# Kernel tuning notes

Measured on AMD Instinct MI355X. Metric: run time of the kernel, lower is better.

The kernel has to match this reference:

```python
import jax, jax.numpy as jnp
import numpy as np

D = 256; NH = 8; NL = 4; NP = 4; DFF = 2048; HD = D // NH
SHAPES = [(64, 64), (32, 32), (16, 16), (8, 8)]
B = 2; LEN = sum(h * w for h, w in SHAPES)


def setup_inputs() -> dict:
    key = jax.random.key(0)
    ks = jax.random.split(key, 12)
    def w(k, shape, s=0.02):
        return jax.random.normal(k, shape, jnp.float32) * s
    starts = np.cumsum([0] + [h * w for h, w in SHAPES[:-1]])
    return {
        "src": jax.random.normal(ks[0], (B, LEN, D), jnp.float32),
        "pos": jax.random.normal(ks[1], (B, LEN, D), jnp.float32) * 0.1,
        "spatial_shapes": jnp.array(SHAPES, dtype=jnp.int32),
        "level_start_index": jnp.array(starts, dtype=jnp.int32),
        "w_value": w(ks[2], (D, D)), "b_value": jnp.zeros((D,), jnp.float32),
        "w_off": w(ks[3], (D, NH * NL * NP * 2)), "b_off": w(ks[4], (NH * NL * NP * 2,), 0.1),
        "w_attn": w(ks[5], (D, NH * NL * NP)), "b_attn": jnp.zeros((NH * NL * NP,), jnp.float32),
        "w_out": w(ks[6], (D, D)), "b_out": jnp.zeros((D,), jnp.float32),
        "w1": w(ks[7], (D, DFF)), "b1": jnp.zeros((DFF,), jnp.float32),
        "w2": w(ks[8], (DFF, D)), "b2": jnp.zeros((D,), jnp.float32),
        "g1": jnp.ones((D,), jnp.float32), "be1": jnp.zeros((D,), jnp.float32),
        "g2": jnp.ones((D,), jnp.float32), "be2": jnp.zeros((D,), jnp.float32),
    }


def _layer_norm(x, g, b):
    mu = jnp.mean(x, -1, keepdims=True)
    v = jnp.var(x, -1, keepdims=True)
    return (x - mu) * jax.lax.rsqrt(v + 1e-5) * g + b


def _reference_points(shapes):
    # torch.linspace(0.5, H-0.5, H)/H == (arange(H)+0.5)/H
    refs = []
    for H, W in shapes:
        ry = (jnp.arange(H, dtype=jnp.float32) + 0.5) / H
        rx = (jnp.arange(W, dtype=jnp.float32) + 0.5) / W
        yy, xx = jnp.meshgrid(ry, rx, indexing='ij')
        refs.append(jnp.stack([xx.ravel(), yy.ravel()], -1))
    return jnp.concatenate(refs, 0)  # (Len, 2) as (x, y)


def _ms_deform_sample(value, loc, shapes):
    # value: (B, Len, NH, HD); loc: (B, Lq, NH, NL, NP, 2) normalized [0,1]
    # Replicates torch grid_sample(bilinear, padding='zeros', align_corners=False).
    Bn, Lq = loc.shape[0], loc.shape[1]
    P = loc.shape[4]
    start = 0
    outs = []
    for lvl, (H, W) in enumerate(shapes):
        v = value[:, start:start + H * W].transpose(0, 2, 1, 3)  # (B, NH, HW, HD)
        start += H * W
        l = loc[:, :, :, lvl]                      # (B, Lq, NH, P, 2)
        x = l[..., 0] * W - 0.5
        y = l[..., 1] * H - 0.5
        x0 = jnp.floor(x); y0 = jnp.floor(y)
        dx = x - x0; dy = y - y0
        x0i = x0.astype(jnp.int32); y0i = y0.astype(jnp.int32)
        acc = None
        for xi, yi, wgt in ((x0i, y0i, (1 - dx) * (1 - dy)),
                            (x0i + 1, y0i, dx * (1 - dy)),
                            (x0i, y0i + 1, (1 - dx) * dy),
                            (x0i + 1, y0i + 1, dx * dy)):
            valid = ((xi >= 0) & (xi < W) & (yi >= 0) & (yi < H)).astype(value.dtype)
            idx = jnp.clip(yi, 0, H - 1) * W + jnp.clip(xi, 0, W - 1)  # (B, Lq, NH, P)
            idx = idx.transpose(0, 2, 1, 3).reshape(Bn, NH, Lq * P)
            g = jnp.take_along_axis(v, idx[..., None], axis=2).reshape(Bn, NH, Lq, P, HD)
            w = (wgt * valid).transpose(0, 2, 1, 3)[..., None]  # (B, NH, Lq, P, 1)
            acc = g * w if acc is None else acc + g * w
        outs.append(acc)  # (B, NH, Lq, P, HD)
    return jnp.stack(outs, 3)  # (B, NH, Lq, NL, NP, HD)


def _forward(src, pos, w_value, b_value, w_off, b_off, w_attn, b_attn,
             w_out, b_out, w1, b1, w2, b2, g1, be1, g2, be2, shapes):
    Bn, Lq, _ = src.shape
    q = src + pos  # with_pos_embed
    value = (src @ w_value + b_value).reshape(Bn, Lq, NH, HD)
    off = (q @ w_off + b_off).reshape(Bn, Lq, NH, NL, NP, 2)
    attn = jax.nn.softmax((q @ w_attn + b_attn).reshape(Bn, Lq, NH, NL * NP), -1)
    attn = attn.reshape(Bn, Lq, NH, NL, NP)
    ref = _reference_points(shapes)  # (Len, 2)
    normalizer = jnp.array([[w_, h_] for h_, w_ in shapes], jnp.float32)  # (NL, 2) = (W, H)
    loc = ref[None, :, None, None, None, :] + off / normalizer[None, None, None, :, None, :]
    sampled = _ms_deform_sample(value, loc, shapes)  # (B, NH, Lq, NL, NP, HD)
    out = jnp.einsum('bqhlp,bhqlpd->bqhd', attn, sampled).reshape(Bn, Lq, D)
    out = out @ w_out + b_out
    x = _layer_norm(src + out, g1, be1)           # residual + norm1
    ff = jax.nn.relu(x @ w1 + b1) @ w2 + b2       # FFN (dropout=0)
    return _layer_norm(x + ff, g2, be2)           # residual + norm2


def reference(src, pos, spatial_shapes, level_start_index, w_value, b_value,
              w_off, b_off, w_attn, b_attn, w_out, b_out, w1, b1, w2, b2,
              g1, be1, g2, be2):
    shapes = [tuple(int(v) for v in s) for s in np.asarray(spatial_shapes)]
    return _forward(src, pos, w_value, b_value, w_off, b_off, w_attn, b_attn,
                    w_out, b_out, w1, b1, w2, b2, g1, be1, g2, be2, shapes)
```

## Files before the change

### kernel.cpp

```cpp
#include <hip/hip_runtime.h>
#include <math.h>

#define D 256
#define NH 8
#define NL 4
#define NP 4
#define DFF 2048
#define HD 32
#define BB 2
#define LEN 5440
#define MROWS (BB * LEN)

typedef __attribute__((ext_vector_type(8))) short short8;
typedef __attribute__((ext_vector_type(4))) float f32x4;
typedef unsigned int uint32;

__device__ __forceinline__ unsigned short f2bf(float f) {
    uint32 u = __float_as_uint(f);
    u += 0x7FFF + ((u >> 16) & 1);
    return (unsigned short)(u >> 16);
}
__device__ __forceinline__ float bf2f(unsigned short h) {
    return __uint_as_float(((uint32)h) << 16);
}
__device__ __forceinline__ uint32 pack2(float a, float b) {
    return (uint32)f2bf(a) | ((uint32)f2bf(b) << 16);
}
__device__ __forceinline__ void acc8(float* a, uint4 u, float w) {
    a[0] += bf2f((unsigned short)u.x) * w; a[1] += bf2f((unsigned short)(u.x >> 16)) * w;
    a[2] += bf2f((unsigned short)u.y) * w; a[3] += bf2f((unsigned short)(u.y >> 16)) * w;
    a[4] += bf2f((unsigned short)u.z) * w; a[5] += bf2f((unsigned short)(u.z >> 16)) * w;
    a[6] += bf2f((unsigned short)u.w) * w; a[7] += bf2f((unsigned short)(u.w >> 16)) * w;
}

__device__ __forceinline__ void gl16(const unsigned short* g, unsigned short* l) {
    __builtin_amdgcn_global_load_lds(
        (const __attribute__((address_space(1))) unsigned int*)g,
        (__attribute__((address_space(3))) unsigned int*)l, 16, 0, 0);
}

__device__ __forceinline__ void swz85(int b, int ncols, int& row, int& col) {
    const int gsz = ncols << 3;
    const int full = 10 * gsz;
    if (b < full) {
        const int g = b / gsz, idx = b - g * gsz;
        row = (g << 3) + (idx & 7);
        col = idx >> 3;
    } else {
        const int idx = b - full;
        row = 80 + idx % 5;
        col = idx / 5;
    }
}

__global__ void prep_a(const float* __restrict__ w_value, const float* __restrict__ w_off,
                       const float* __restrict__ w_attn,
                       const float* __restrict__ b_value, const float* __restrict__ b_off,
                       const float* __restrict__ b_attn,
                       unsigned short* __restrict__ wqvT, float* __restrict__ bqv) {
    __shared__ float tile[32][33];
    const int blk = blockIdx.x;
    const int t = threadIdx.x;
    if (blk >= 160) {
        for (int i = t; i < 640; i += 256)
            bqv[i] = (i < 256) ? b_value[i] : (i < 512 ? b_off[i - 256] : b_attn[i - 512]);
        return;
    }
    const float* W; unsigned short* WT; int N, tid;
    if (blk < 64)       { W = w_value; WT = wqvT;             N = 256; tid = blk; }
    else if (blk < 128) { W = w_off;   WT = wqvT + 256 * 256; N = 256; tid = blk - 64; }
    else                { W = w_attn;  WT = wqvT + 512 * 256; N = 128; tid = blk - 128; }
    const int K = 256;
    const int ntx = N >> 5;
    const int nb = (tid % ntx) * 32, kb = (tid / ntx) * 32;
    const int tx = t & 31, ty = t >> 5;
#pragma unroll
    for (int i = 0; i < 32; i += 8)
        tile[ty + i][tx] = W[(size_t)(kb + ty + i) * N + nb + tx];
    __syncthreads();
#pragma unroll
    for (int i = 0; i < 32; i += 8)
        WT[(size_t)(nb + ty + i) * K + kb + tx] = f2bf(tile[tx][ty + i]);
}

__global__ __launch_bounds__(256) void ffn1_gemm(
        const unsigned short* __restrict__ A,
        const unsigned short* __restrict__ BT, const float* __restrict__ bias,
        unsigned short* __restrict__ Cv, int N, int K, int lda, int ldb) {
    __shared__ unsigned short smraw[17408];
    auto Ash = (unsigned short (*)[128][32])smraw;
    auto Bsh = (unsigned short (*)[128][32])(smraw + 8192);

    int rowt, colt;
    swz85(blockIdx.x, N >> 7, rowt, colt);
    const int row0 = rowt * 128, col0 = colt * 128;

    const int t = threadIdx.x;
    const int wave = t >> 6, lane = t & 63;
    const int wr = wave >> 1, wc = wave & 1;
    const int lrow = lane & 15, quad = lane >> 4;
    const int sr = lane >> 2, sc = (lane & 3) * 8;

    const unsigned short* Ab = A + (size_t)row0 * lda;
    const unsigned short* Bb = BT + (size_t)col0 * ldb;

    f32x4 acc[4][4];
#pragma unroll
    for (int i = 0; i < 4; i++)
#pragma unroll
        for (int j = 0; j < 4; j++) acc[i][j] = (f32x4){0.f, 0.f, 0.f, 0.f};

    auto stage = [&](int buf, int kb) {
#pragma unroll
        for (int j = 0; j < 2; j++) {
            const int r = wave * 32 + j * 16;
            gl16(Ab + (size_t)(r + sr) * lda + kb + sc, &Ash[buf][r][0]);
            gl16(Bb + (size_t)(r + sr) * ldb + kb + sc, &Bsh[buf][r][0]);
        }
    };

    stage(0, 0);
    int i = 0;
    for (int kb = 0; kb < K; kb += 32, ++i) {
        __syncthreads();
        if (kb + 32 < K) stage((i + 1) & 1, kb + 32);
        const int cf = i & 1;
        short8 af[4], bfr[4];
#pragma unroll
        for (int mt = 0; mt < 4; mt++)
            af[mt] = *(const short8*)&Ash[cf][wr * 64 + mt * 16 + lrow][quad * 8];
#pragma unroll
        for (int nt = 0; nt < 4; nt++)
            bfr[nt] = *(const short8*)&Bsh[cf][wc * 64 + nt * 16 + lrow][quad * 8];
#pragma unroll
        for (int mt = 0; mt < 4; mt++)
#pragma unroll
            for (int nt = 0; nt < 4; nt++)
                acc[mt][nt] = __builtin_amdgcn_mfma_f32_16x16x32_bf16(
                    af[mt], bfr[nt], acc[mt][nt], 0, 0, 0);
    }

    __syncthreads();
    auto bounce = (unsigned short (*)[136])smraw;
#pragma unroll
    for (int nt = 0; nt < 4; nt++) {
        const int cl = wc * 64 + nt * 16 + lrow;
        const float bv = bias[col0 + cl];
#pragma unroll
        for (int mt = 0; mt < 4; mt++) {
            f32x4 a = acc[mt][nt];
#pragma unroll
            for (int r = 0; r < 4; r++)
                bounce[wr * 64 + mt * 16 + quad * 4 + r][cl] = f2bf(fmaxf(a[r] + bv, 0.f));
        }
    }
    __syncthreads();
#pragma unroll
    for (int pass = 0; pass < 8; pass++) {
        const int rl = pass * 16 + (t >> 4), ch = t & 15;
        *(uint4*)&Cv[(size_t)(row0 + rl) * N + col0 + ch * 8] =
            *(const uint4*)&bounce[rl][ch * 8];
    }
}

template <int NZ>
__global__ __launch_bounds__(256) void splitk_gemm(
        const unsigned short* __restrict__ A, const unsigned short* __restrict__ BT,
        unsigned short* __restrict__ part, int KC, int lda, int ldb) {
    __shared__ unsigned short smraw[17408];
    auto Ash = (unsigned short (*)[128][32])smraw;
    auto Bsh = (unsigned short (*)[128][32])(smraw + 8192);

    int rowt, cc;
    swz85(blockIdx.x, 2 * NZ, rowt, cc);
    const int row0 = rowt * 128;
    const int col0 = (cc & 1) * 128;
    const int z = cc >> 1;
    const int koff = z * KC;
    unsigned short* __restrict__ C = part + (size_t)z * MROWS * 256;

    const int t = threadIdx.x;
    const int wave = t >> 6, lane = t & 63;
    const int wr = wave >> 1, wc = wave & 1;
    const int lrow = lane & 15, quad = lane >> 4;
    const int sr = lane >> 2, sc = (lane & 3) * 8;

    const unsigned short* Ab = A + (size_t)row0 * lda + koff;
    const unsigned short* Bb = BT + (size_t)col0 * ldb + koff;

    f32x4 acc[4][4];
#pragma unroll
    for (int i = 0; i < 4; i++)
#pragma unroll
        for (int j = 0; j < 4; j++) acc[i][j] = (f32x4){0.f, 0.f, 0.f, 0.f};

    auto stage = [&](int buf, int kb) {
#pragma unroll
        for (int j = 0; j < 2; j++) {
            const int r = wave * 32 + j * 16;
            gl16(Ab + (size_t)(r + sr) * lda + kb + sc, &Ash[buf][r][0]);
            gl16(Bb + (size_t)(r + sr) * ldb + kb + sc, &Bsh[buf][r][0]);
        }
    };

    stage(0, 0);
    int i = 0;
    for (int kb = 0; kb < KC; kb += 32, ++i) {
        __syncthreads();
        if (kb + 32 < KC) stage((i + 1) & 1, kb + 32);
        const int cf = i & 1;
        short8 af[4], bfr[4];
#pragma unroll
        for (int mt = 0; mt < 4; mt++)
            af[mt] = *(const short8*)&Ash[cf][wr * 64 + mt * 16 + lrow][quad * 8];
#pragma unroll
        for (int nt = 0; nt < 4; nt++)
            bfr[nt] = *(const short8*)&Bsh[cf][wc * 64 + nt * 16 + lrow][quad * 8];
#pragma unroll
        for (int mt = 0; mt < 4; mt++)
#pragma unroll
            for (int nt = 0; nt < 4; nt++)
                acc[mt][nt] = __builtin_amdgcn_mfma_f32_16x16x32_bf16(
                    af[mt], bfr[nt], acc[mt][nt], 0, 0, 0);
    }

    __syncthreads();
    auto bounce = (unsigned short (*)[136])smraw;
#pragma unroll
    for (int nt = 0; nt < 4; nt++) {
        const int cl = wc * 64 + nt * 16 + lrow;
#pragma unroll
        for (int mt = 0; mt < 4; mt++) {
            f32x4 a = acc[mt][nt];
#pragma unroll
            for (int r = 0; r < 4; r++)
                bounce[wr * 64 + mt * 16 + quad * 4 + r][cl] = f2bf(a[r]);
        }
    }
    __syncthreads();
#pragma unroll
    for (int pass = 0; pass < 8; pass++) {
        const int rl = pass * 16 + (t >> 4), ch = t & 15;
        *(uint4*)&C[(size_t)(row0 + rl) * 256 + col0 + ch * 8] =
            *(const uint4*)&bounce[rl][ch * 8];
    }
}

__global__ __launch_bounds__(256) void gemm_ln(
        const unsigned short* __restrict__ A, const unsigned short* __restrict__ BT,
        const float* __restrict__ bias, const float* __restrict__ rsd,
        const float* __restrict__ g, const float* __restrict__ be,
        unsigned short* __restrict__ out16, int K) {
    __shared__ unsigned short Ash[2][32][32];
    __shared__ unsigned short Bsh[2][256][32];
    __shared__ float red1[4][32], red2[4][32];

    const int row0 = blockIdx.x * 32;
    const int t = threadIdx.x;
    const int wave = t >> 6, lane = t & 63;
    const int lrow = lane & 15, quad = lane >> 4;
    const int sr = lane >> 2, sc = (lane & 3) * 8;

    f32x4 acc[2][4];
#pragma unroll
    for (int i = 0; i < 2; i++)
#pragma unroll
        for (int j = 0; j < 4; j++) acc[i][j] = (f32x4){0.f, 0.f, 0.f, 0.f};

    auto stage = [&](int buf, int kb) {
#pragma unroll
        for (int j = 0; j < 4; j++) {
            const int r = wave * 64 + j * 16;
            gl16(BT + (size_t)(r + sr) * K + kb + sc, &Bsh[buf][r][0]);
        }
        if (wave < 2) {
            const int r = wave * 16;
            gl16(A + (size_t)(row0 + r + sr) * K + kb + sc, &Ash[buf][r][0]);
        }
    };

    stage(0, 0);
    int it = 0;
    for (int kb = 0; kb < K; kb += 32, ++it) {
        __syncthreads();
        if (kb + 32 < K) stage((it + 1) & 1, kb + 32);
        const int cf = it & 1;
        short8 af[2], bfr[4];
#pragma unroll
        for (int mt = 0; mt < 2; mt++)
            af[mt] = *(const short8*)&Ash[cf][mt * 16 + lrow][quad * 8];
#pragma unroll
        for (int nt = 0; nt < 4; nt++)
            bfr[nt] = *(const short8*)&Bsh[cf][wave * 64 + nt * 16 + lrow][quad * 8];
#pragma unroll
        for (int mt = 0; mt < 2; mt++)
#pragma unroll
            for (int nt = 0; nt < 4; nt++)
                acc[mt][nt] = __builtin_amdgcn_mfma_f32_16x16x32_bf16(
                    af[mt], bfr[nt], acc[mt][nt], 0, 0, 0);
    }

    float gv[4], bev[4], bv[4];
#pragma unroll
    for (int nt = 0; nt < 4; nt++) {
        const int col = wave * 64 + nt * 16 + lrow;
        bv[nt] = bias[col];
        gv[nt] = g[col];
        bev[nt] = be[col];
    }

    float v[2][4][4];
#pragma unroll
    for (int mt = 0; mt < 2; mt++)
#pragma unroll
        for (int r = 0; r < 4; r++) {
            const int row = row0 + mt * 16 + quad * 4 + r;
#pragma unroll
            for (int nt = 0; nt < 4; nt++) {
                const int col = wave * 64 + nt * 16 + lrow;
                v[mt][nt][r] = acc[mt][nt][r] + bv[nt] + rsd[(size_t)row * 256 + col];
            }
        }

#pragma unroll
    for (int mt = 0; mt < 2; mt++)
#pragma unroll
        for (int r = 0; r < 4; r++) {
            float s1 = v[mt][0][r] + v[mt][1][r] + v[mt][2][r] + v[mt][3][r];
            float s2 = v[mt][0][r] * v[mt][0][r] + v[mt][1][r] * v[mt][1][r] +
                       v[mt][2][r] * v[mt][2][r] + v[mt][3][r] * v[mt][3][r];
#pragma unroll
            for (int o = 1; o < 16; o <<= 1) {
                s1 += __shfl_xor(s1, o, 16);
                s2 += __shfl_xor(s2, o, 16);
            }
            if (lrow == 0) {
                const int rr = mt * 16 + quad * 4 + r;
                red1[wave][rr] = s1;
                red2[wave][rr] = s2;
            }
        }
    __syncthreads();

#pragma unroll
    for (int mt = 0; mt < 2; mt++)
#pragma unroll
        for (int r = 0; r < 4; r++) {
            const int rr = mt * 16 + quad * 4 + r;
            const float su = red1[0][rr] + red1[1][rr] + red1[2][rr] + red1[3][rr];
            const float sq = red2[0][rr] + red2[1][rr] + red2[2][rr] + red2[3][rr];
            const float mean = su * (1.0f / 256.0f);
            const float var = fmaxf(sq * (1.0f / 256.0f) - mean * mean, 0.f);
            const float rstd = rsqrtf(var + 1e-5f);
            const size_t rowoff = (size_t)(row0 + rr) * 256;
#pragma unroll
            for (int nt = 0; nt < 4; nt++) {
                const int col = wave * 64 + nt * 16 + lrow;
                const float o = (v[mt][nt][r] - mean) * rstd * gv[nt] + bev[nt];
                out16[rowoff + col] = f2bf(o);
            }
        }
}

__global__ __launch_bounds__(256) void qv_gemm(
        const float* __restrict__ src, const float* __restrict__ pos,
        const unsigned short* __restrict__ BT, const float* __restrict__ bias,
        unsigned short* __restrict__ val, unsigned short* __restrict__ qout16) {
    __shared__ unsigned short smraw[18432];
    auto Ash = (unsigned short (*)[128][40])smraw;
    auto Bsh = (unsigned short (*)[128][32])(smraw + 10240);

    int rowt, colt;
    swz85(blockIdx.x, 5, rowt, colt);
    const int row0 = rowt * 128, col0 = colt * 128;
    const bool addp = (col0 >= 256);

    const int t = threadIdx.x;
    const int wave = t >> 6, lane = t & 63;
    const int wr = wave >> 1, wc = wave & 1;
    const int lrow = lane & 15, quad = lane >> 4;
    const int srow = t >> 1;
    const int cb = (t & 1) * 16;
    const int sr = lane >> 2, sc = (lane & 3) * 8;

    const float* ap = src + (size_t)(row0 + srow) * 256 + cb;
    const float* pp = pos + (size_t)(row0 + srow) * 256 + cb;
    const unsigned short* Bb = BT + (size_t)col0 * 256;

    f32x4 acc[4][4];
#pragma unroll
    for (int i = 0; i < 4; i++)
#pragma unroll
        for (int j = 0; j < 4; j++) acc[i][j] = (f32x4){0.f, 0.f, 0.f, 0.f};

    float4 fa[4]; float4 fp[4];
    auto packA = [&](int buf) {
        float4 f0 = fa[0], f1 = fa[1], f2 = fa[2], f3 = fa[3];
        if (addp) {
            f0.x += fp[0].x; f0.y += fp[0].y; f0.z += fp[0].z; f0.w += fp[0].w;
            f1.x += fp[1].x; f1.y += fp[1].y; f1.z += fp[1].z; f1.w += fp[1].w;
            f2.x += fp[2].x; f2.y += fp[2].y; f2.z += fp[2].z; f2.w += fp[2].w;
            f3.x += fp[3].x; f3.y += fp[3].y; f3.z += fp[3].z; f3.w += fp[3].w;
        }
        uint4 u0 = make_uint4(pack2(f0.x, f0.y), pack2(f0.z, f0.w),
                              pack2(f1.x, f1.y), pack2(f1.z, f1.w));
        uint4 u1 = make_uint4(pack2(f2.x, f2.y), pack2(f2.z, f2.w),
                              pack2(f3.x, f3.y), pack2(f3.z, f3.w));
        *(uint4*)&Ash[buf][srow][cb + 0] = u0;
        *(uint4*)&Ash[buf][srow][cb + 8] = u1;
    };
    auto loadA = [&](int kb) {
#pragma unroll
        for (int j = 0; j < 4; j++) fa[j] = *(const float4*)(ap + kb + 4 * j);
        if (addp) {
#pragma unroll
            for (int j = 0; j < 4; j++) fp[j] = *(const float4*)(pp + kb + 4 * j);
        }
    };
    auto stageB = [&](int buf, int kb) {
#pragma unroll
        for (int j = 0; j < 2; j++) {
            const int r = wave * 32 + j * 16;
            gl16(Bb + (size_t)(r + sr) * 256 + kb + sc, &Bsh[buf][r][0]);
        }
    };

    loadA(0);
    packA(0);
    stageB(0, 0);
    loadA(32);

    int i = 0;
    for (int kb = 0; kb < 256; kb += 32, ++i) {
        __syncthreads();
        if (kb + 32 < 256) {
            stageB((i + 1) & 1, kb + 32);
            packA((i + 1) & 1);
            if (kb + 64 < 256) loadA(kb + 64);
        }
        const int cf = i & 1;
        short8 af[4], bfr[4];
#pragma unroll
        for (int mt = 0; mt < 4; mt++)
            af[mt] = *(const short8*)&Ash[cf][wr * 64 + mt * 16 + lrow][quad * 8];
#pragma unroll
        for (int nt = 0; nt < 4; nt++)
            bfr[nt] = *(const short8*)&Bsh[cf][wc * 64 + nt * 16 + lrow][quad * 8];
#pragma unroll
        for (int mt = 0; mt < 4; mt++)
#pragma unroll
            for (int nt = 0; nt < 4; nt++)
                acc[mt][nt] = __builtin_amdgcn_mfma_f32_16x16x32_bf16(
                    af[mt], bfr[nt], acc[mt][nt], 0, 0, 0);
    }

    __syncthreads();
    auto bounce = (unsigned short (*)[136])smraw;
#pragma unroll
    for (int nt = 0; nt < 4; nt++) {
        const int cl = wc * 64 + nt * 16 + lrow;
        const float bv = bias[col0 + cl];
#pragma unroll
        for (int mt = 0; mt < 4; mt++) {
            f32x4 a = acc[mt][nt];
#pragma unroll
            for (int r = 0; r < 4; r++)
                bounce[wr * 64 + mt * 16 + quad * 4 + r][cl] = f2bf(a[r] + bv);
        }
    }
    __syncthreads();
    unsigned short* Cp; int ldc, c0;
    if (col0 < 256) { Cp = val;    ldc = 256; c0 = col0; }
    else            { Cp = qout16; ldc = 384; c0 = col0 - 256; }
#pragma unroll
    for (int pass = 0; pass < 8; pass++) {
        const int rl = pass * 16 + (t >> 4), ch = t & 15;
        *(uint4*)&Cp[(size_t)(row0 + rl) * ldc + c0 + ch * 8] =
            *(const uint4*)&bounce[rl][ch * 8];
    }
}

__global__ void sampler(const unsigned short* __restrict__ val,
                        const unsigned short* __restrict__ qout16,
                        unsigned short* __restrict__ out,
                        const float* __restrict__ w_out, const float* __restrict__ w1,
                        const float* __restrict__ w2,
                        unsigned short* __restrict__ woT, unsigned short* __restrict__ w1T,
                        unsigned short* __restrict__ w2T) {
    __shared__ __align__(16) int   sIdx[4][128][4];
    __shared__ __align__(16) float sW[4][128][4];
    __shared__ float tileT[32][33];
    const int t = threadIdx.x;

    if (blockIdx.x >= MROWS / 4) {
        const int bk = (int)blockIdx.x - MROWS / 4;
        const float* W; unsigned short* WT; int K, N, tid;
        if (bk < 64)       { W = w_out; WT = woT;  K = 256;  N = 256;  tid = bk; }
        else if (bk < 576) { W = w1;    WT = w1T;  K = 256;  N = 2048; tid = bk - 64; }
        else               { W = w2;    WT = w2T;  K = 2048; N = 256;  tid = bk - 576; }
        const int ntx = N >> 5;
        const int nb = (tid % ntx) * 32, kb = (tid / ntx) * 32;
        const int tx = t & 31, ty = t >> 5;
#pragma unroll
        for (int i = 0; i < 32; i += 8)
            tileT[ty + i][tx] = W[(size_t)(kb + ty + i) * N + nb + tx];
        __syncthreads();
#pragma unroll
        for (int i = 0; i < 32; i += 8)
            WT[(size_t)(nb + ty + i) * K + kb + tx] = f2bf(tileT[tx][ty + i]);
        return;
    }

    const int pair = t & 127;
    const int qsel = t >> 7;
    const int h1 = pair >> 4, p1 = pair & 15;
    const int lvl = p1 >> 2;

#pragma unroll
    for (int j = 0; j < 2; j++) {
        const int ql = qsel + 2 * j;
        const int bq = (int)blockIdx.x * 4 + ql;
        const int b = bq / LEN, q = bq % LEN;

        float refx, refy;
        if (q < 4096) {
            int rq = q >> 6, cq = q & 63;
            refx = (cq + 0.5f) * (1.0f / 64.0f);
            refy = (rq + 0.5f) * (1.0f / 64.0f);
        } else if (q < 5120) {
            int qq = q - 4096;
            int rq = qq >> 5, cq = qq & 31;
            refx = (cq + 0.5f) * (1.0f / 32.0f);
            refy = (rq + 0.5f) * (1.0f / 32.0f);
        } else if (q < 5376) {
            int qq = q - 5120;
            int rq = qq >> 4, cq = qq & 15;
            refx = (cq + 0.5f) * (1.0f / 16.0f);
            refy = (rq + 0.5f) * (1.0f / 16.0f);
        } else {
            int qq = q - 5376;
            int rq = qq >> 3, cq = qq & 7;
            refx = (cq + 0.5f) * (1.0f / 8.0f);
            refy = (rq + 0.5f) * (1.0f / 8.0f);
        }

        float lv = bf2f(qout16[(size_t)bq * 384 + 256 + pair]);
        float mx = lv;
#pragma unroll
        for (int o = 1; o < 16; o <<= 1) mx = fmaxf(mx, __shfl_xor(mx, o, 16));
        float e = expf(lv - mx);
        float s = e;
#pragma unroll
        for (int o = 1; o < 16; o <<= 1) s += __shfl_xor(s, o, 16);
        const float aw = e / s;

        const uint32 opair = *(const uint32*)&qout16[(size_t)bq * 384 + h1 * 32 + p1 * 2];
        const float ox = bf2f((unsigned short)opair);
        const float oy = bf2f((unsigned short)(opair >> 16));

        const int LST[4] = {0, 4096, 5120, 5376};
        const int WW = 64 >> lvl;
        const float rw = 1.0f / (float)WW;

        float x = (refx + ox * rw) * (float)WW - 0.5f;
        float y = (refy + oy * rw) * (float)WW - 0.5f;
        float x0f = floorf(x), y0f = floorf(y);
        float dx = x - x0f, dy = y - y0f;
        int x0 = (int)x0f, y0 = (int)y0f;

        const int base = (b * LEN + LST[lvl]) * 256 + h1 * 32;
        int xs[2] = {x0, x0 + 1}, ys[2] = {y0, y0 + 1};
        float wx[2] = {1.f - dx, dx}, wy[2] = {1.f - dy, dy};
        int ic[4]; float wc4[4];
#pragma unroll
        for (int cy = 0; cy < 2; cy++)
#pragma unroll
            for (int cx = 0; cx < 2; cx++) {
                int xi = xs[cx], yi = ys[cy];
                bool vld = (xi >= 0) && (xi < WW) && (yi >= 0) && (yi < WW);
                int xc = min(max(xi, 0), WW - 1);
                int yc = min(max(yi, 0), WW - 1);
                ic[cy * 2 + cx] = base + (yc * WW + xc) * 256;
                wc4[cy * 2 + cx] = vld ? wx[cx] * wy[cy] * aw : 0.f;
            }
        *(int4*)&sIdx[ql][pair][0] = make_int4(ic[0], ic[1], ic[2], ic[3]);
        *(float4*)&sW[ql][pair][0] = make_float4(wc4[0], wc4[1], wc4[2], wc4[3]);
    }
    __syncthreads();

    const int g = t >> 6;
    const int l6 = t & 63;
    const int h = l6 >> 3;
    const int chg = l6 & 3;
    const int ph = (l6 >> 2) & 1;
    const int bq = (int)blockIdx.x * 4 + g;
    const unsigned short* vald = val + chg * 8;
    float a[8];
#pragma unroll
    for (int c = 0; c < 8; c++) a[c] = 0.f;
#pragma unroll
    for (int pi = 0; pi < 8; pi++) {
        const int r = h * 16 + ph * 8 + pi;
        int4 iv = *(const int4*)&sIdx[g][r][0];
        float4 wv = *(const float4*)&sW[g][r][0];
        uint4 u0 = *(const uint4*)(vald + iv.x);
        uint4 u1 = *(const uint4*)(vald + iv.y);
        uint4 u2 = *(const uint4*)(vald + iv.z);
        uint4 u3 = *(const uint4*)(vald + iv.w);
        acc8(a, u0, wv.x); acc8(a, u1, wv.y); acc8(a, u2, wv.z); acc8(a, u3, wv.w);
    }
#pragma unroll
    for (int c = 0; c < 8; c++) a[c] += __shfl_xor(a[c], 4, 64);
    if (ph == 0) {
        uint4 o;
        o.x = pack2(a[0], a[1]); o.y = pack2(a[2], a[3]);
        o.z = pack2(a[4], a[5]); o.w = pack2(a[6], a[7]);
        *(uint4*)&out[(size_t)bq * D + h * HD + chg * 8] = o;
    }
}

__global__ void add_ln4(const unsigned short* __restrict__ part16,
                        const float* __restrict__ bias,
                        const unsigned short* __restrict__ rsd16,
                        const float* __restrict__ g, const float* __restrict__ be,
                        float* __restrict__ out) {
    const int wave = threadIdx.x >> 6, lane = threadIdx.x & 63;
    const int row = blockIdx.x * 4 + wave;
    const int c0 = lane * 4;
    const size_t i = (size_t)row * 256 + c0;

    float v[4];
    {
        ushort4 r = *(const ushort4*)&rsd16[i];
        float4 bv = *(const float4*)&bias[c0];
        v[0] = bf2f(r.x) + bv.x; v[1] = bf2f(r.y) + bv.y;
        v[2] = bf2f(r.z) + bv.z; v[3] = bf2f(r.w) + bv.w;
    }
#pragma unroll
    for (int z = 0; z < 4; z++) {
        ushort4 p = *(const ushort4*)&part16[(size_t)z * MROWS * 256 + i];
        v[0] += bf2f(p.x); v[1] += bf2f(p.y); v[2] += bf2f(p.z); v[3] += bf2f(p.w);
    }
    float s1 = v[0] + v[1] + v[2] + v[3];
    float s2 = v[0] * v[0] + v[1] * v[1] + v[2] * v[2] + v[3] * v[3];
#pragma unroll
    for (int o = 32; o > 0; o >>= 1) {
        s1 += __shfl_xor(s1, o, 64);
        s2 += __shfl_xor(s2, o, 64);
    }
    const float mean = s1 * (1.0f / 256.0f);
    const float var = fmaxf(s2 * (1.0f / 256.0f) - mean * mean, 0.f);
    const float rstd = rsqrtf(var + 1e-5f);

    float4 gv = *(const float4*)&g[c0];
    float4 bev = *(const float4*)&be[c0];
    float4 o4;
    o4.x = (v[0] - mean) * rstd * gv.x + bev.x;
    o4.y = (v[1] - mean) * rstd * gv.y + bev.y;
    o4.z = (v[2] - mean) * rstd * gv.z + bev.z;
    o4.w = (v[3] - mean) * rstd * gv.w + bev.w;
    *(float4*)&out[i] = o4;
}

extern "C" void kernel_launch(void* const* d_in, const int* in_sizes, int n_in,
                              void* d_out, int out_size, void* d_ws, size_t ws_size,
                              hipStream_t stream) {
    const float* src     = (const float*)d_in[0];
    const float* pos     = (const float*)d_in[1];
    const float* w_value = (const float*)d_in[4];
    const float* b_value = (const float*)d_in[5];
    const float* w_off   = (const float*)d_in[6];
    const float* b_off   = (const float*)d_in[7];
    const float* w_attn  = (const float*)d_in[8];
    const float* b_attn  = (const float*)d_in[9];
    const float* w_out   = (const float*)d_in[10];
    const float* b_out   = (const float*)d_in[11];
    const float* w1      = (const float*)d_in[12];
    const float* b1      = (const float*)d_in[13];
    const float* w2      = (const float*)d_in[14];
    const float* b2      = (const float*)d_in[15];
    const float* g1      = (const float*)d_in[16];
    const float* be1     = (const float*)d_in[17];
    const float* g2      = (const float*)d_in[18];
    const float* be2     = (const float*)d_in[19];
    float* out = (float*)d_out;

    size_t off = 0;
    auto alloc = [&](size_t bytes) -> char* {
        char* p = (char*)d_ws + off;
        off += (bytes + 255) & ~(size_t)255;
        return p;
    };
    unsigned short* wqvT = (unsigned short*)alloc((size_t)640 * 256 * 2);
    unsigned short* woT  = (unsigned short*)alloc(256 * 256 * 2);
    unsigned short* w1T  = (unsigned short*)alloc((size_t)2048 * 256 * 2);
    unsigned short* w2T  = (unsigned short*)alloc((size_t)256 * 2048 * 2);
    float* bqv           = (float*)alloc(640 * 4);

    unsigned short* qout = (unsigned short*)alloc((size_t)MROWS * 384 * 2);
    unsigned short* val  = (unsigned short*)alloc((size_t)MROWS * 256 * 2);
    unsigned short* attn = (unsigned short*)alloc((size_t)MROWS * 256 * 2);
    unsigned short* hb   = (unsigned short*)alloc((size_t)MROWS * 2048 * 2);
    unsigned short* xb16 = (unsigned short*)alloc((size_t)MROWS * 256 * 2);
    unsigned short* part = (unsigned short*)alloc((size_t)4 * MROWS * 256 * 2);

    prep_a<<<161, 256, 0, stream>>>(w_value, w_off, w_attn, b_value, b_off, b_attn,
                                    wqvT, bqv);

    qv_gemm<<<425, 256, 0, stream>>>(src, pos, wqvT, bqv, val, qout);
    sampler<<<MROWS / 4 + 1088, 256, 0, stream>>>(val, qout, attn,
                                                  w_out, w1, w2, woT, w1T, w2T);
    gemm_ln<<<340, 256, 0, stream>>>(attn, woT, b_out, src, g1, be1, xb16, 256);

    ffn1_gemm<<<1360, 256, 0, stream>>>(xb16, w1T, b1, hb, 2048, 256, 256, 256);
    splitk_gemm<4><<<680, 256, 0, stream>>>(hb, w2T, part, 512, 2048, 2048);
    add_ln4<<<MROWS / 4, 256, 0, stream>>>(part, b2, xb16, g2, be2, out);
}
```

Before: 194.8 us.

## Fuse FFN up- and down-projection into one kernel with split-K partials

```diff
diff --git a/kernel.cpp b/kernel.cpp
--- a/kernel.cpp
+++ b/kernel.cpp
@@ -83,17 +83,21 @@
         WT[(size_t)(nb + ty + i) * K + kb + tx] = f2bf(tile[tx][ty + i]);
 }
 
-__global__ __launch_bounds__(256) void ffn1_gemm(
+__global__ __launch_bounds__(256, 2) void ffn_fused(
         const unsigned short* __restrict__ A,
-        const unsigned short* __restrict__ BT, const float* __restrict__ bias,
-        unsigned short* __restrict__ Cv, int N, int K, int lda, int ldb) {
-    __shared__ unsigned short smraw[17408];
-    auto Ash = (unsigned short (*)[128][32])smraw;
-    auto Bsh = (unsigned short (*)[128][32])(smraw + 8192);
-
-    int rowt, colt;
-    swz85(blockIdx.x, N >> 7, rowt, colt);
-    const int row0 = rowt * 128, col0 = colt * 128;
+        const unsigned short* __restrict__ w1T,
+        const float* __restrict__ b1,
+        const unsigned short* __restrict__ w2T,
+        unsigned short* __restrict__ part) {
+    __shared__ __align__(16) unsigned short smraw[32768];
+    unsigned short* Hsh = smraw;
+    auto Ash = (unsigned short (*)[128][32])(smraw + 16384);
+    auto Bsh = (unsigned short (*)[128][32])(smraw + 24576);
+
+    int rowt, s;
+    swz85(blockIdx.x, 8, rowt, s);
+    const int row0 = rowt * 128;
+    const int hb0 = s * 256;
 
     const int t = threadIdx.x;
     const int wave = t >> 6, lane = t & 63;
@@ -101,148 +105,132 @@
     const int lrow = lane & 15, quad = lane >> 4;
     const int sr = lane >> 2, sc = (lane & 3) * 8;
 
-    const unsigned short* Ab = A + (size_t)row0 * lda;
-    const unsigned short* Bb = BT + (size_t)col0 * ldb;
-
-    f32x4 acc[4][4];
-#pragma unroll
-    for (int i = 0; i < 4; i++)
-#pragma unroll
-        for (int j = 0; j < 4; j++) acc[i][j] = (f32x4){0.f, 0.f, 0.f, 0.f};
-
-    auto stage = [&](int buf, int kb) {
-#pragma unroll
-        for (int j = 0; j < 2; j++) {
-            const int r = wave * 32 + j * 16;
-            gl16(Ab + (size_t)(r + sr) * lda + kb + sc, &Ash[buf][r][0]);
-            gl16(Bb + (size_t)(r + sr) * ldb + kb + sc, &Bsh[buf][r][0]);
-        }
-    };
-
-    stage(0, 0);
-    int i = 0;
-    for (int kb = 0; kb < K; kb += 32, ++i) {
+    f32x4 acc2[2][4][4];
+#pragma unroll
+    for (int o = 0; o < 2; o++)
+#pragma unroll
+        for (int i = 0; i < 4; i++)
+#pragma unroll
+            for (int j = 0; j < 4; j++) acc2[o][i][j] = (f32x4){0.f, 0.f, 0.f, 0.f};
+
+    const unsigned short* Ab = A + (size_t)row0 * 256;
+
+    for (int hc = 0; hc < 2; hc++) {
+        const unsigned short* Bb = w1T + (size_t)(hb0 + hc * 128) * 256;
+        f32x4 acc1[4][4];
+#pragma unroll
+        for (int i = 0; i < 4; i++)
+#pragma unroll
+            for (int j = 0; j < 4; j++) acc1[i][j] = (f32x4){0.f, 0.f, 0.f, 0.f};
+
+        auto stage1 = [&](int buf, int kb) {
+#pragma unroll
+            for (int j = 0; j < 2; j++) {
+                const int r = wave * 32 + j * 16;
+                gl16(Ab + (size_t)(r + sr) * 256 + kb + sc, &Ash[buf][r][0]);
+                gl16(Bb + (size_t)(r + sr) * 256 + kb + sc, &Bsh[buf][r][0]);
+            }
+        };
+        stage1(0, 0);
+        int it = 0;
+        for (int kb = 0; kb < 256; kb += 32, ++it) {
+            __syncthreads();
+            if (kb + 32 < 256) stage1((it + 1) & 1, kb + 32);
+            const int cf = it & 1;
+            short8 af[4], bfr[4];
+#pragma unroll
+            for (int mt = 0; mt < 4; mt++)
+                af[mt] = *(const short8*)&Ash[cf][wr * 64 + mt * 16 + lrow][quad * 8];
+#pragma unroll
+            for (int nt = 0; nt < 4; nt++)
+                bfr[nt] = *(const short8*)&Bsh[cf][wc * 64 + nt * 16 + lrow][quad * 8];
+#pragma unroll
+            for (int mt = 0; mt < 4; mt++)
+#pragma unroll
+                for (int nt = 0; nt < 4; nt++)
+                    acc1[mt][nt] = __builtin_amdgcn_mfma_f32_16x16x32_bf16(
+                        af[mt], bfr[nt], acc1[mt][nt], 0, 0, 0);
+        }
+
+#pragma unroll
+        for (int nt = 0; nt < 4; nt++) {
+            const int col = wc * 64 + nt * 16 + lrow;
+            const float bv = b1[hb0 + hc * 128 + col];
+#pragma unroll
+            for (int mt = 0; mt < 4; mt++) {
+                f32x4 a = acc1[mt][nt];
+#pragma unroll
+                for (int r = 0; r < 4; r++) {
+                    const int row = wr * 64 + mt * 16 + quad * 4 + r;
+                    Hsh[row * 128 + (col ^ ((row & 7) << 3))] =
+                        f2bf(fmaxf(a[r] + bv, 0.f));
+                }
+            }
+        }
         __syncthreads();
-        if (kb + 32 < K) stage((i + 1) & 1, kb + 32);
-        const int cf = i & 1;
-        short8 af[4], bfr[4];
-#pragma unroll
-        for (int mt = 0; mt < 4; mt++)
-            af[mt] = *(const short8*)&Ash[cf][wr * 64 + mt * 16 + lrow][quad * 8];
-#pragma unroll
-        for (int nt = 0; nt < 4; nt++)
-            bfr[nt] = *(const short8*)&Bsh[cf][wc * 64 + nt * 16 + lrow][quad * 8];
-#pragma unroll
-        for (int mt = 0; mt < 4; mt++)
-#pragma unroll
-            for (int nt = 0; nt < 4; nt++)
-                acc[mt][nt] = __builtin_amdgcn_mfma_f32_16x16x32_bf16(
-                    af[mt], bfr[nt], acc[mt][nt], 0, 0, 0);
-    }
-
-    __syncthreads();
-    auto bounce = (unsigned short (*)[136])smraw;
-#pragma unroll
-    for (int nt = 0; nt < 4; nt++) {
-        const int cl = wc * 64 + nt * 16 + lrow;
-        const float bv = bias[col0 + cl];
-#pragma unroll
-        for (int mt = 0; mt < 4; mt++) {
-            f32x4 a = acc[mt][nt];
-#pragma unroll
-            for (int r = 0; r < 4; r++)
-                bounce[wr * 64 + mt * 16 + quad * 4 + r][cl] = f2bf(fmaxf(a[r] + bv, 0.f));
-        }
-    }
-    __syncthreads();
-#pragma unroll
-    for (int pass = 0; pass < 8; pass++) {
-        const int rl = pass * 16 + (t >> 4), ch = t & 15;
-        *(uint4*)&Cv[(size_t)(row0 + rl) * N + col0 + ch * 8] =
-            *(const uint4*)&bounce[rl][ch * 8];
-    }
-}
-
-template <int NZ>
-__global__ __launch_bounds__(256) void splitk_gemm(
-        const unsigned short* __restrict__ A, const unsigned short* __restrict__ BT,
-        unsigned short* __restrict__ part, int KC, int lda, int ldb) {
-    __shared__ unsigned short smraw[17408];
-    auto Ash = (unsigned short (*)[128][32])smraw;
-    auto Bsh = (unsigned short (*)[128][32])(smraw + 8192);
-
-    int rowt, cc;
-    swz85(blockIdx.x, 2 * NZ, rowt, cc);
-    const int row0 = rowt * 128;
-    const int col0 = (cc & 1) * 128;
-    const int z = cc >> 1;
-    const int koff = z * KC;
-    unsigned short* __restrict__ C = part + (size_t)z * MROWS * 256;
-
-    const int t = threadIdx.x;
-    const int wave = t >> 6, lane = t & 63;
-    const int wr = wave >> 1, wc = wave & 1;
-    const int lrow = lane & 15, quad = lane >> 4;
-    const int sr = lane >> 2, sc = (lane & 3) * 8;
-
-    const unsigned short* Ab = A + (size_t)row0 * lda + koff;
-    const unsigned short* Bb = BT + (size_t)col0 * ldb + koff;
-
-    f32x4 acc[4][4];
-#pragma unroll
-    for (int i = 0; i < 4; i++)
-#pragma unroll
-        for (int j = 0; j < 4; j++) acc[i][j] = (f32x4){0.f, 0.f, 0.f, 0.f};
-
-    auto stage = [&](int buf, int kb) {
-#pragma unroll
-        for (int j = 0; j < 2; j++) {
-            const int r = wave * 32 + j * 16;
-            gl16(Ab + (size_t)(r + sr) * lda + kb + sc, &Ash[buf][r][0]);
-            gl16(Bb + (size_t)(r + sr) * ldb + kb + sc, &Bsh[buf][r][0]);
-        }
-    };
-
-    stage(0, 0);
-    int i = 0;
-    for (int kb = 0; kb < KC; kb += 32, ++i) {
+
+#pragma unroll
+        for (int oc = 0; oc < 2; oc++) {
+            const unsigned short* B2 = w2T + (size_t)(oc * 128) * 2048 + hb0 + hc * 128;
+            auto stage2 = [&](int buf, int kb) {
+#pragma unroll
+                for (int j = 0; j < 2; j++) {
+                    const int r = wave * 32 + j * 16;
+                    gl16(B2 + (size_t)(r + sr) * 2048 + kb + sc, &Bsh[buf][r][0]);
+                }
+            };
+            stage2(0, 0);
+            int it2 = 0;
+            for (int kb = 0; kb < 128; kb += 32, ++it2) {
+                __syncthreads();
+                if (kb + 32 < 128) stage2((it2 + 1) & 1, kb + 32);
+                const int cf = it2 & 1;
+                short8 af[4], bfr[4];
+#pragma unroll
+                for (int mt = 0; mt < 4; mt++) {
+                    const int row = wr * 64 + mt * 16 + lrow;
+                    af[mt] = *(const short8*)
+                        &Hsh[row * 128 + ((kb + quad * 8) ^ ((row & 7) << 3))];
+                }
+#pragma unroll
+                for (int nt = 0; nt < 4; nt++)
+                    bfr[nt] = *(const short8*)&Bsh[cf][wc * 64 + nt * 16 + lrow][quad * 8];
+#pragma unroll
+                for (int mt = 0; mt < 4; mt++)
+#pragma unroll
+                    for (int nt = 0; nt < 4; nt++)
+                        acc2[oc][mt][nt] = __builtin_amdgcn_mfma_f32_16x16x32_bf16(
+                            af[mt], bfr[nt], acc2[oc][mt][nt], 0, 0, 0);
+            }
+            __syncthreads();
+        }
+    }
+
+    unsigned short* C = part + (size_t)s * MROWS * 256;
+    unsigned short* bnc = smraw + 16384;
+#pragma unroll
+    for (int oc = 0; oc < 2; oc++) {
+#pragma unroll
+        for (int nt = 0; nt < 4; nt++) {
+            const int col = wc * 64 + nt * 16 + lrow;
+#pragma unroll
+            for (int mt = 0; mt < 4; mt++) {
+                f32x4 a = acc2[oc][mt][nt];
+#pragma unroll
+                for (int r = 0; r < 4; r++) {
+                    const int row = wr * 64 + mt * 16 + quad * 4 + r;
+                    bnc[row * 128 + (col ^ ((row & 7) << 3))] = f2bf(a[r]);
+                }
+            }
+        }
         __syncthreads();
-        if (kb + 32 < KC) stage((i + 1) & 1, kb + 32);
-        const int cf = i & 1;
-        short8 af[4], bfr[4];
-#pragma unroll
-        for (int mt = 0; mt < 4; mt++)
-            af[mt] = *(const short8*)&Ash[cf][wr * 64 + mt * 16 + lrow][quad * 8];
-#pragma unroll
-        for (int nt = 0; nt < 4; nt++)
-            bfr[nt] = *(const short8*)&Bsh[cf][wc * 64 + nt * 16 + lrow][quad * 8];
-#pragma unroll
-        for (int mt = 0; mt < 4; mt++)
-#pragma unroll
-            for (int nt = 0; nt < 4; nt++)
-                acc[mt][nt] = __builtin_amdgcn_mfma_f32_16x16x32_bf16(
-                    af[mt], bfr[nt], acc[mt][nt], 0, 0, 0);
-    }
-
-    __syncthreads();
-    auto bounce = (unsigned short (*)[136])smraw;
-#pragma unroll
-    for (int nt = 0; nt < 4; nt++) {
-        const int cl = wc * 64 + nt * 16 + lrow;
-#pragma unroll
-        for (int mt = 0; mt < 4; mt++) {
-            f32x4 a = acc[mt][nt];
-#pragma unroll
-            for (int r = 0; r < 4; r++)
-                bounce[wr * 64 + mt * 16 + quad * 4 + r][cl] = f2bf(a[r]);
-        }
-    }
-    __syncthreads();
-#pragma unroll
-    for (int pass = 0; pass < 8; pass++) {
-        const int rl = pass * 16 + (t >> 4), ch = t & 15;
-        *(uint4*)&C[(size_t)(row0 + rl) * 256 + col0 + ch * 8] =
-            *(const uint4*)&bounce[rl][ch * 8];
+#pragma unroll
+        for (int pass = 0; pass < 8; pass++) {
+            const int rl = pass * 16 + (t >> 4), ch = t & 15;
+            *(uint4*)&C[(size_t)(row0 + rl) * 256 + oc * 128 + ch * 8] =
+                *(const uint4*)&bnc[rl * 128 + ((ch * 8) ^ ((rl & 7) << 3))];
+        }
+        __syncthreads();
     }
 }
 
@@ -619,7 +607,7 @@
     }
 }
 
-__global__ void add_ln4(const unsigned short* __restrict__ part16,
+__global__ void add_ln8(const unsigned short* __restrict__ part16,
                         const float* __restrict__ bias,
                         const unsigned short* __restrict__ rsd16,
                         const float* __restrict__ g, const float* __restrict__ be,
@@ -637,7 +625,7 @@
         v[2] = bf2f(r.z) + bv.z; v[3] = bf2f(r.w) + bv.w;
     }
 #pragma unroll
-    for (int z = 0; z < 4; z++) {
+    for (int z = 0; z < 8; z++) {
         ushort4 p = *(const ushort4*)&part16[(size_t)z * MROWS * 256 + i];
         v[0] += bf2f(p.x); v[1] += bf2f(p.y); v[2] += bf2f(p.z); v[3] += bf2f(p.w);
     }
@@ -700,9 +688,8 @@
     unsigned short* qout = (unsigned short*)alloc((size_t)MROWS * 384 * 2);
     unsigned short* val  = (unsigned short*)alloc((size_t)MROWS * 256 * 2);
     unsigned short* attn = (unsigned short*)alloc((size_t)MROWS * 256 * 2);
-    unsigned short* hb   = (unsigned short*)alloc((size_t)MROWS * 2048 * 2);
     unsigned short* xb16 = (unsigned short*)alloc((size_t)MROWS * 256 * 2);
-    unsigned short* part = (unsigned short*)alloc((size_t)4 * MROWS * 256 * 2);
+    unsigned short* part = (unsigned short*)alloc((size_t)8 * MROWS * 256 * 2);
 
     prep_a<<<161, 256, 0, stream>>>(w_value, w_off, w_attn, b_value, b_off, b_attn,
                                     wqvT, bqv);
@@ -712,7 +699,6 @@
                                                   w_out, w1, w2, woT, w1T, w2T);
     gemm_ln<<<340, 256, 0, stream>>>(attn, woT, b_out, src, g1, be1, xb16, 256);
 
-    ffn1_gemm<<<1360, 256, 0, stream>>>(xb16, w1T, b1, hb, 2048, 256, 256, 256);
-    splitk_gemm<4><<<680, 256, 0, stream>>>(hb, w2T, part, 512, 2048, 2048);
-    add_ln4<<<MROWS / 4, 256, 0, stream>>>(part, b2, xb16, g2, be2, out);
-}
+    ffn_fused<<<680, 256, 0, stream>>>(xb16, w1T, b1, w2T, part);
+    add_ln8<<<MROWS / 4, 256, 0, stream>>>(part, b2, xb16, g2, be2, out);
+}
```

Measured after the change: 272.3 us. +39.8%, slower.
